# Kernel optimization log

Measured on AMD Instinct MI355X. Metric: run time of the kernel, lower is better.

Reference implementation:

```python
import jax, jax.numpy as jnp
import numpy as np

N = 50000      # n_nodes
E = 800000     # n_edges (nnz)
F = 256        # n_features
H = 256        # architecture (GCN hidden)
K = 16         # n_clusters
CLUSTER_REG = 1.0
CON_REG = 1.0


def setup_inputs() -> dict:
    key = jax.random.key(0)
    ks = jax.random.split(key, 12)
    inp = {
        "edge_src": jax.random.randint(ks[0], (E,), 0, N, dtype=jnp.int32),
        "edge_dst": jax.random.randint(ks[1], (E,), 0, N, dtype=jnp.int32),
        "edge_w_norm": jax.random.uniform(ks[2], (E,), dtype=jnp.float32),
        "features": jax.random.normal(ks[3], (N, F), dtype=jnp.float32),
        "aug_features": jax.random.normal(ks[4], (N, F), dtype=jnp.float32),
        # GCN encoder params (Linear no-bias + additive bias per DGI-style GCN)
        "W1": jax.random.normal(ks[5], (F, H), dtype=jnp.float32) / np.sqrt(F),
        "b1": jnp.zeros((H,), dtype=jnp.float32),
        # student GCN params
        "Ws": jax.random.normal(ks[6], (H, K), dtype=jnp.float32) / np.sqrt(H),
        "bs": jnp.zeros((K,), dtype=jnp.float32),
        # teacher GCN params (EMA copy; fixed here)
        "Wt": jax.random.normal(ks[7], (H, K), dtype=jnp.float32) / np.sqrt(H),
        "bt": jnp.zeros((K,), dtype=jnp.float32),
        "n_nodes": N,
    }
    return inp


def _spmm(w, src, dst, X, n):
    # (sparse A) @ X with A given as COO (src=row, dst=col, w=value)
    return jax.ops.segment_sum(w[:, None] * X[dst], src, num_segments=n)


def _gcn(X, W, b, w, src, dst, n):
    # act(spmm(A_norm, X @ W) + b) with act = selu
    return jax.nn.selu(_spmm(w, src, dst, X @ W, n) + b)


def _normalize(x):
    # F.normalize(x, dim=-1, p=2)
    nrm = jnp.sqrt(jnp.sum(x * x, axis=-1, keepdims=True))
    return x / jnp.maximum(nrm, 1e-12)


def reference(edge_src, edge_dst, edge_w_norm, features, aug_features,
              W1, b1, Ws, bs, Wt, bt, n_nodes):
    n = features.shape[0]
    n_edges = edge_src.shape[0]

    # encoder + student assignments
    gcn_out = _gcn(features, W1, b1, edge_w_norm, edge_src, edge_dst, n)
    logits = _spmm(edge_w_norm, edge_src, edge_dst, gcn_out @ Ws, n) + bs
    assignments = jax.nn.softmax(jax.nn.selu(logits), axis=1)  # [N, K]

    # degrees = torch.sparse.sum(graph, dim=0) (binary adjacency values)
    ones_e = jnp.ones((n_edges,), dtype=features.dtype)
    degrees = jax.ops.segment_sum(ones_e, edge_dst, num_segments=n)[:, None]  # [N,1]

    # graph_pooled = (A @ S).T @ S  (A values are all 1)
    AS = jax.ops.segment_sum(assignments[edge_dst], edge_src, num_segments=n)
    graph_pooled = AS.T @ assignments  # [K, K]

    normalizer_left = assignments.T @ degrees          # [K, 1]
    normalizer = (normalizer_left @ normalizer_left.T) / 2.0 / n_edges
    spectral_loss = -jnp.trace(graph_pooled - normalizer) / 2.0 / n_edges

    cluster_sizes = jnp.sum(assignments, axis=0)
    cluster_loss = (jnp.linalg.norm(cluster_sizes) / n_nodes * np.sqrt(float(K)) - 1.0)
    cluster_loss = cluster_loss * CLUSTER_REG

    # teacher branch (no grad)
    g2 = _gcn(aug_features, W1, b1, edge_w_norm, edge_src, edge_dst, n)
    t_logits = _spmm(edge_w_norm, edge_src, edge_dst, g2 @ Wt, n) + bt
    assignments_hat = jax.lax.stop_gradient(
        jax.nn.softmax(jax.nn.selu(t_logits), axis=-1))

    con = jnp.mean(2.0 - 2.0 * jnp.sum(_normalize(assignments_hat) * _normalize(assignments), axis=-1))

    loss = spectral_loss + cluster_loss + CON_REG * con
    return loss
```

## Files before the change

kernel.cpp:

```cpp
#include <hip/hip_runtime.h>
#include <math.h>

constexpr int Fdim = 256;
constexpr int Hdim = 256;
constexpr int Kc   = 16;

constexpr int RSTRIDE = 32;
constexpr int NRED    = 34;
constexpr int BCAP    = 5120;

typedef __attribute__((ext_vector_type(8))) short s8v;
typedef __attribute__((ext_vector_type(4))) float f4v;

__device__ __forceinline__ float selu1(float x){
    const float scale = 1.0507009873554805f;
    const float alpha = 1.6732632423543772f;
    return scale * (x > 0.f ? x : alpha * expm1f(x));
}

__device__ __forceinline__ ushort f2bf(float x){
    union { float f; unsigned u; } c; c.f = x;
    unsigned r = c.u + 0x7fffu + ((c.u >> 16) & 1u);
    return (ushort)(r >> 16);
}

__device__ __forceinline__ float bflo(unsigned v){
    union { unsigned u; float f; } c; c.u = v << 16; return c.f;
}
__device__ __forceinline__ float bfhi(unsigned v){
    union { unsigned u; float f; } c; c.u = v & 0xffff0000u; return c.f;
}

__device__ __forceinline__ unsigned char f2fp8(float x){
    int v = __builtin_amdgcn_cvt_pk_fp8_f32(x, x, 0, false);
    return (unsigned char)(v & 0xff);
}

__global__ __launch_bounds__(256) void bin_kernel(
        const int* __restrict__ src, const int* __restrict__ dst,
        const float* __restrict__ w,
        int* __restrict__ bcnt,
        int* __restrict__ bsrc, uint2* __restrict__ bdw, int E, int nbuck){
    __shared__ int hist[256];
    __shared__ int base[256];
    __shared__ int cur[256];
    int t = threadIdx.x;
    int chunk = (E + gridDim.x - 1) / gridDim.x;
    int lo = blockIdx.x * chunk;
    int hi = min(lo + chunk, E);
    hist[t] = 0;
    __syncthreads();
    for (int i = lo + t; i < hi; i += 256)
        atomicAdd(&hist[src[i] >> 8], 1);
    __syncthreads();
    if (t < nbuck && hist[t] > 0)
        base[t] = atomicAdd(&bcnt[t * 32], hist[t]);
    cur[t] = 0;
    __syncthreads();
    for (int i = lo + t; i < hi; i += 256){
        int s = src[i], d = dst[i];
        float wv = w[i];
        int b = s >> 8;
        int p = base[b] + atomicAdd(&cur[b], 1);
        if (p < BCAP){
            bsrc[(size_t)b * BCAP + p] = s;
            bdw[(size_t)b * BCAP + p]  = make_uint2((unsigned)d, __float_as_uint(wv));
        }
    }
}

__global__ __launch_bounds__(256) void bbase_kernel(const int* __restrict__ bcnt,
        int* __restrict__ bbase, int* __restrict__ roff, int nbuck, int n){
    __shared__ int s[256];
    int t = threadIdx.x;
    int v = (t < nbuck) ? min(bcnt[t * 32], BCAP) : 0;
    s[t] = v;
    __syncthreads();
    for (int off = 1; off < 256; off <<= 1){
        int x = (t >= off) ? s[t - off] : 0;
        __syncthreads();
        s[t] += x;
        __syncthreads();
    }
    if (t < nbuck) bbase[t] = s[t] - v;
    if (t == 255) roff[n] = s[255];
}

__global__ __launch_bounds__(256) void csr_build_kernel(
        const int* __restrict__ bcnt, const int* __restrict__ bbase,
        const int* __restrict__ bsrc, const uint2* __restrict__ bdw,
        int* __restrict__ roff, uint2* __restrict__ csr, int n){
    __shared__ int hist[256];
    __shared__ int loc[256];
    __shared__ int cur[256];
    int b = blockIdx.x, t = threadIdx.x;
    int cnt  = min(bcnt[b * 32], BCAP);
    int base = bbase[b];
    hist[t] = 0;
    __syncthreads();
    for (int i = t; i < cnt; i += 256)
        atomicAdd(&hist[bsrc[(size_t)b * BCAP + i] & 255], 1);
    __syncthreads();
    int v = hist[t];
    loc[t] = v;
    __syncthreads();
    for (int off = 1; off < 256; off <<= 1){
        int x = (t >= off) ? loc[t - off] : 0;
        __syncthreads();
        loc[t] += x;
        __syncthreads();
    }
    int gi = b * 256 + t;
    if (gi < n) roff[gi] = base + loc[t] - v;
    cur[t] = 0;
    __syncthreads();
    for (int i = t; i < cnt; i += 256){
        int s   = bsrc[(size_t)b * BCAP + i];
        int idx = s & 255;
        int p = base + (loc[idx] - hist[idx]) + atomicAdd(&cur[idx], 1);
        csr[p] = bdw[(size_t)b * BCAP + i];
    }
}

__global__ void castw_kernel(const float* __restrict__ W, ushort* __restrict__ Wt){
    __shared__ float t[16][17];
    int tx = threadIdx.x, ty = threadIdx.y;
    int k  = blockIdx.y * 16 + ty;
    int nn = blockIdx.x * 16 + tx;
    t[ty][tx] = W[k * 256 + nn];
    __syncthreads();
    int n2 = blockIdx.x * 16 + ty;
    int k2 = blockIdx.y * 16 + tx;
    Wt[n2 * 256 + k2] = f2bf(t[tx][ty]);
}

__global__ void castwk_kernel(const float* __restrict__ Ws, const float* __restrict__ Wt,
                              ushort* __restrict__ WsT, ushort* __restrict__ WtT){
    int h = threadIdx.x;
    #pragma unroll
    for (int c = 0; c < 16; ++c){
        WsT[c * 256 + h] = f2bf(Ws[h * 16 + c]);
        WtT[c * 256 + h] = f2bf(Wt[h * 16 + c]);
    }
}

__global__ __launch_bounds__(256, 2) void gemm_xw_kernel(
        const float* __restrict__ A0, const float* __restrict__ A1,
        const ushort* __restrict__ Bt,
        unsigned char* __restrict__ C8, int M){
    __shared__ ushort blds[32768];
    int tid = threadIdx.x;
    int n0  = blockIdx.x * 128;
    int bm  = blockIdx.y * 128;
    const float* A = blockIdx.z ? A1 : A0;
    int halfoff = blockIdx.z * 256;

    #pragma unroll
    for (int j = 0; j < 16; ++j){
        int c  = j * 256 + tid;
        int nl = c >> 5, kc = c & 31;
        uint4 v = *reinterpret_cast<const uint4*>(Bt + (((size_t)(n0 + nl)) << 8) + (kc << 3));
        unsigned boff = (unsigned)(((nl << 9) + (kc << 4)) ^ ((nl & 7) << 4));
        *reinterpret_cast<uint4*>(reinterpret_cast<char*>(blds) + boff) = v;
    }

    int w = tid >> 6, l = tid & 63;
    int lr = l & 15, lk = l >> 4;

    int r0 = bm + w * 32 + lr;
    int r1 = r0 + 16;
    int rc0 = min(r0, M - 1), rc1 = min(r1, M - 1);
    const float* a0 = A + (size_t)rc0 * 256 + lk * 8;
    const float* a1 = A + (size_t)rc1 * 256 + lk * 8;

    float4 f[16], g[16];
    #pragma unroll
    for (int ks = 0; ks < 8; ++ks){
        f[2*ks]   = *reinterpret_cast<const float4*>(a0 + ks * 32);
        f[2*ks+1] = *reinterpret_cast<const float4*>(a0 + ks * 32 + 4);
        g[2*ks]   = *reinterpret_cast<const float4*>(a1 + ks * 32);
        g[2*ks+1] = *reinterpret_cast<const float4*>(a1 + ks * 32 + 4);
    }
    s8v af0[8], af1[8];
    #pragma unroll
    for (int ks = 0; ks < 8; ++ks){
        float4 x0 = f[2*ks], x1 = f[2*ks+1];
        af0[ks][0] = (short)f2bf(x0.x); af0[ks][1] = (short)f2bf(x0.y);
        af0[ks][2] = (short)f2bf(x0.z); af0[ks][3] = (short)f2bf(x0.w);
        af0[ks][4] = (short)f2bf(x1.x); af0[ks][5] = (short)f2bf(x1.y);
        af0[ks][6] = (short)f2bf(x1.z); af0[ks][7] = (short)f2bf(x1.w);
        float4 y0 = g[2*ks], y1 = g[2*ks+1];
        af1[ks][0] = (short)f2bf(y0.x); af1[ks][1] = (short)f2bf(y0.y);
        af1[ks][2] = (short)f2bf(y0.z); af1[ks][3] = (short)f2bf(y0.w);
        af1[ks][4] = (short)f2bf(y1.x); af1[ks][5] = (short)f2bf(y1.y);
        af1[ks][6] = (short)f2bf(y1.z); af1[ks][7] = (short)f2bf(y1.w);
    }
    __syncthreads();

    f4v acc[2][8];
    #pragma unroll
    for (int m = 0; m < 2; ++m)
        #pragma unroll
        for (int t = 0; t < 8; ++t)
            acc[m][t] = (f4v){0.f, 0.f, 0.f, 0.f};

    #pragma unroll
    for (int ks = 0; ks < 8; ++ks){
        #pragma unroll
        for (int t = 0; t < 8; ++t){
            int nl = t * 16 + lr;
            unsigned boff = (unsigned)(((nl << 9) + ((ks * 4 + lk) << 4)) ^ ((nl & 7) << 4));
            s8v bf = *reinterpret_cast<const s8v*>(reinterpret_cast<const char*>(blds) + boff);
            acc[0][t] = __builtin_amdgcn_mfma_f32_16x16x32_bf16(af0[ks], bf, acc[0][t], 0, 0, 0);
            acc[1][t] = __builtin_amdgcn_mfma_f32_16x16x32_bf16(af1[ks], bf, acc[1][t], 0, 0, 0);
        }
    }

    #pragma unroll
    for (int m = 0; m < 2; ++m){
        #pragma unroll
        for (int t = 0; t < 8; ++t){
            int col = n0 + t * 16 + lr;
            #pragma unroll
            for (int j = 0; j < 4; ++j){
                int row = bm + w * 32 + m * 16 + lk * 4 + j;
                if (row < M) C8[(size_t)row * 512 + halfoff + col] = f2fp8(acc[m][t][j]);
            }
        }
    }
}

__global__ __launch_bounds__(256) void spmm_h2_kernel(
        const unsigned char* __restrict__ XWp,
        const int* __restrict__ roff, const uint2* __restrict__ csr,
        const float* __restrict__ b1,
        ushort* __restrict__ Gs, ushort* __restrict__ Gt, int n){
    int wid = threadIdx.x >> 6, lane = threadIdx.x & 63;
    int r = blockIdx.x * 4 + wid;
    if (r >= n) return;
    int half = lane >> 5;
    int hl   = lane & 31;
    const unsigned char* base = XWp + lane * 8;
    int e0 = roff[r], e1 = roff[r + 1];
    float acc[8] = {};

    #define ACCUM8(V, W) do{                                                      \
        auto fa_ = __builtin_amdgcn_cvt_pk_f32_fp8((V).x, false);                 \
        acc[0] = fmaf((W), fa_[0], acc[0]); acc[1] = fmaf((W), fa_[1], acc[1]);   \
        auto fb_ = __builtin_amdgcn_cvt_pk_f32_fp8((V).x, true);                  \
        acc[2] = fmaf((W), fb_[0], acc[2]); acc[3] = fmaf((W), fb_[1], acc[3]);   \
        auto fc_ = __builtin_amdgcn_cvt_pk_f32_fp8((V).y, false);                 \
        acc[4] = fmaf((W), fc_[0], acc[4]); acc[5] = fmaf((W), fc_[1], acc[5]);   \
        auto fd_ = __builtin_amdgcn_cvt_pk_f32_fp8((V).y, true);                  \
        acc[6] = fmaf((W), fd_[0], acc[6]); acc[7] = fmaf((W), fd_[1], acc[7]);   \
    }while(0)

    int e = e0;
    for (; e + 7 < e1; e += 8){
        uint2 c0 = csr[e],     c1 = csr[e + 1];
        uint2 c2 = csr[e + 2], c3 = csr[e + 3];
        uint2 c4 = csr[e + 4], c5 = csr[e + 5];
        uint2 c6 = csr[e + 6], c7 = csr[e + 7];
        uint2 v0 = *reinterpret_cast<const uint2*>(base + ((size_t)c0.x << 9));
        uint2 v1 = *reinterpret_cast<const uint2*>(base + ((size_t)c1.x << 9));
        uint2 v2 = *reinterpret_cast<const uint2*>(base + ((size_t)c2.x << 9));
        uint2 v3 = *reinterpret_cast<const uint2*>(base + ((size_t)c3.x << 9));
        uint2 v4 = *reinterpret_cast<const uint2*>(base + ((size_t)c4.x << 9));
        uint2 v5 = *reinterpret_cast<const uint2*>(base + ((size_t)c5.x << 9));
        uint2 v6 = *reinterpret_cast<const uint2*>(base + ((size_t)c6.x << 9));
        uint2 v7 = *reinterpret_cast<const uint2*>(base + ((size_t)c7.x << 9));
        ACCUM8(v0, __uint_as_float(c0.y)); ACCUM8(v1, __uint_as_float(c1.y));
        ACCUM8(v2, __uint_as_float(c2.y)); ACCUM8(v3, __uint_as_float(c3.y));
        ACCUM8(v4, __uint_as_float(c4.y)); ACCUM8(v5, __uint_as_float(c5.y));
        ACCUM8(v6, __uint_as_float(c6.y)); ACCUM8(v7, __uint_as_float(c7.y));
    }
    for (; e + 3 < e1; e += 4){
        uint2 c0 = csr[e],     c1 = csr[e + 1];
        uint2 c2 = csr[e + 2], c3 = csr[e + 3];
        uint2 v0 = *reinterpret_cast<const uint2*>(base + ((size_t)c0.x << 9));
        uint2 v1 = *reinterpret_cast<const uint2*>(base + ((size_t)c1.x << 9));
        uint2 v2 = *reinterpret_cast<const uint2*>(base + ((size_t)c2.x << 9));
        uint2 v3 = *reinterpret_cast<const uint2*>(base + ((size_t)c3.x << 9));
        ACCUM8(v0, __uint_as_float(c0.y)); ACCUM8(v1, __uint_as_float(c1.y));
        ACCUM8(v2, __uint_as_float(c2.y)); ACCUM8(v3, __uint_as_float(c3.y));
    }
    for (; e < e1; ++e){
        uint2 c = csr[e];
        uint2 v = *reinterpret_cast<const uint2*>(base + ((size_t)c.x << 9));
        ACCUM8(v, __uint_as_float(c.y));
    }
    #undef ACCUM8

    const float* bp = b1 + hl * 8;
    float4 bb0 = *reinterpret_cast<const float4*>(bp);
    float4 bb1 = *reinterpret_cast<const float4*>(bp + 4);
    float bv[8] = {bb0.x, bb0.y, bb0.z, bb0.w, bb1.x, bb1.y, bb1.z, bb1.w};
    ushort o[8];
    #pragma unroll
    for (int q = 0; q < 8; ++q) o[q] = f2bf(selu1(acc[q] + bv[q]));
    uint4 ov = *reinterpret_cast<const uint4*>(o);
    ushort* gout = (half ? Gt : Gs) + (size_t)r * Hdim + hl * 8;
    *reinterpret_cast<uint4*>(gout) = ov;
}

__global__ __launch_bounds__(256) void gemm_k2_kernel(
        const ushort* __restrict__ Gs, const ushort* __restrict__ Gt,
        const ushort* __restrict__ WsT, const ushort* __restrict__ WtT,
        unsigned* __restrict__ GSp, int n){
    int wv = blockIdx.x * 4 + (threadIdx.x >> 6);
    int l  = threadIdx.x & 63;
    int lr = l & 15, lk = l >> 4;
    int nw = (n + 15) >> 4;
    if (wv >= nw) return;
    int r0 = wv * 16;

    s8v bs_[8], bt_[8];
    #pragma unroll
    for (int ks = 0; ks < 8; ++ks){
        bs_[ks] = *reinterpret_cast<const s8v*>(WsT + lr * 256 + ks * 32 + lk * 8);
        bt_[ks] = *reinterpret_cast<const s8v*>(WtT + lr * 256 + ks * 32 + lk * 8);
    }

    f4v accs = (f4v){0.f,0.f,0.f,0.f}, acct = (f4v){0.f,0.f,0.f,0.f};
    int row = min(r0 + lr, n - 1);
    const ushort* gsrow = Gs + (size_t)row * 256 + lk * 8;
    const ushort* gtrow = Gt + (size_t)row * 256 + lk * 8;
    #pragma unroll
    for (int ks = 0; ks < 8; ++ks){
        s8v a_s = *reinterpret_cast<const s8v*>(gsrow + ks * 32);
        s8v a_t = *reinterpret_cast<const s8v*>(gtrow + ks * 32);
        accs = __builtin_amdgcn_mfma_f32_16x16x32_bf16(a_s, bs_[ks], accs, 0, 0, 0);
        acct = __builtin_amdgcn_mfma_f32_16x16x32_bf16(a_t, bt_[ks], acct, 0, 0, 0);
    }
    #pragma unroll
    for (int j = 0; j < 4; ++j){
        int rr = r0 + lk * 4 + j;
        if (rr < n){
            unsigned pv = (unsigned)f2bf(accs[j]) | ((unsigned)f2bf(acct[j]) << 16);
            GSp[(size_t)rr * 16 + lr] = pv;
        }
    }
}

__global__ __launch_bounds__(256) void spmm_k2_kernel(
        const unsigned* __restrict__ GSp,
        const int* __restrict__ roff, const uint2* __restrict__ csr,
        const float* __restrict__ bsv, const float* __restrict__ btv,
        float* __restrict__ asg, float* __restrict__ red, int n){
    int tid  = threadIdx.x;
    int wid  = tid >> 6, lane = tid & 63;
    int slot = lane >> 4, j = lane & 15;
    float bs_ = bsv[j], bt_ = btv[j];
    float cs_l = 0.f, con_l = 0.f;

    int rstride = gridDim.x * 4;
    for (int r = blockIdx.x * 4 + wid; r < n; r += rstride){
        int e0 = roff[r], e1 = roff[r + 1];
        float as_ = 0.f, at_ = 0.f;
        for (int e = e0 + slot; e < e1; e += 4){
            uint2 c = csr[e];
            float w = __uint_as_float(c.y);
            unsigned v = GSp[(size_t)c.x * 16 + j];
            as_ = fmaf(w, bflo(v), as_);
            at_ = fmaf(w, bfhi(v), at_);
        }
        as_ += __shfl_xor(as_, 16); as_ += __shfl_xor(as_, 32);
        at_ += __shfl_xor(at_, 16); at_ += __shfl_xor(at_, 32);
        float xs = selu1(as_ + bs_);
        float xt = selu1(at_ + bt_);
        float ms = xs, mt = xt;
        #pragma unroll
        for (int off = 8; off >= 1; off >>= 1){
            ms = fmaxf(ms, __shfl_xor(ms, off));
            mt = fmaxf(mt, __shfl_xor(mt, off));
        }
        float es = expf(xs - ms), et = expf(xt - mt);
        float ss = es, st = et;
        #pragma unroll
        for (int off = 8; off >= 1; off >>= 1){
            ss += __shfl_xor(ss, off);
            st += __shfl_xor(st, off);
        }
        float a = es / ss, b = et / st;
        if (slot == 0) asg[(size_t)r * 16 + j] = a;
        cs_l += a;
        float dot = a * b, na = a * a, nb = b * b;
        #pragma unroll
        for (int off = 8; off >= 1; off >>= 1){
            dot += __shfl_xor(dot, off);
            na  += __shfl_xor(na, off);
            nb  += __shfl_xor(nb, off);
        }
        if (j == 0){
            na = fmaxf(sqrtf(na), 1e-12f);
            nb = fmaxf(sqrtf(nb), 1e-12f);
            con_l += 2.f - 2.f * dot / (na * nb);
        }
    }

    cs_l  += __shfl_xor(cs_l, 16);  cs_l  += __shfl_xor(cs_l, 32);  cs_l  *= 0.25f;
    con_l += __shfl_xor(con_l, 16); con_l += __shfl_xor(con_l, 32); con_l *= 0.25f;

    __shared__ float part[4][17];
    if (lane < 16) part[wid][lane] = cs_l;
    if (lane == 0) part[wid][16]   = con_l;
    __syncthreads();
    if (tid < 16){
        float s = part[0][tid] + part[1][tid] + part[2][tid] + part[3][tid];
        atomicAdd(&red[(16 + tid) * RSTRIDE], s);
    } else if (tid == 16){
        float s = part[0][16] + part[1][16] + part[2][16] + part[3][16];
        atomicAdd(&red[32 * RSTRIDE], s);
    }
}

__global__ __launch_bounds__(256) void edge_trace_kernel(const int* __restrict__ src,
        const int* __restrict__ dst, const float* __restrict__ as_,
        float* __restrict__ red, int E){
    int tid    = blockIdx.x * blockDim.x + threadIdx.x;
    int stride = gridDim.x * blockDim.x;
    float dot = 0.f;
    float nl[16] = {};
    for (int i = tid; i < E; i += stride){
        const float4* pa = reinterpret_cast<const float4*>(as_ + (size_t)src[i] * 16);
        const float4* pb = reinterpret_cast<const float4*>(as_ + (size_t)dst[i] * 16);
        #pragma unroll
        for (int q = 0; q < 4; ++q){
            float4 va = pa[q]; float4 vb = pb[q];
            dot = fmaf(va.x, vb.x, dot); dot = fmaf(va.y, vb.y, dot);
            dot = fmaf(va.z, vb.z, dot); dot = fmaf(va.w, vb.w, dot);
            nl[q*4+0] += vb.x; nl[q*4+1] += vb.y;
            nl[q*4+2] += vb.z; nl[q*4+3] += vb.w;
        }
    }
    #pragma unroll
    for (int off = 1; off < 64; off <<= 1){
        dot += __shfl_xor(dot, off);
        #pragma unroll
        for (int k = 0; k < 16; ++k) nl[k] += __shfl_xor(nl[k], off);
    }
    __shared__ float part[4][17];
    int wid = threadIdx.x >> 6, lane = threadIdx.x & 63;
    if (lane == 0){
        #pragma unroll
        for (int k = 0; k < 16; ++k) part[wid][k] = nl[k];
        part[wid][16] = dot;
    }
    __syncthreads();
    int t = threadIdx.x;
    if (t < 16){
        float s = part[0][t] + part[1][t] + part[2][t] + part[3][t];
        atomicAdd(&red[t * RSTRIDE], s);
    } else if (t == 16){
        float s = part[0][16] + part[1][16] + part[2][16] + part[3][16];
        atomicAdd(&red[33 * RSTRIDE], s);
    }
}

__global__ void finalize_kernel(const float* __restrict__ red, float* __restrict__ out,
                                int n, int E){
    float trace = red[33 * RSTRIDE];
    float nl2 = 0.f, cs2 = 0.f;
    #pragma unroll
    for (int k = 0; k < 16; ++k){
        nl2 = fmaf(red[k * RSTRIDE],        red[k * RSTRIDE],        nl2);
        cs2 = fmaf(red[(16 + k) * RSTRIDE], red[(16 + k) * RSTRIDE], cs2);
    }
    float twoE = 2.f * (float)E;
    float spectral = -(trace - nl2 / twoE) / twoE;
    float cluster  = sqrtf(cs2) / (float)n * 4.f - 1.f;
    float con      = red[32 * RSTRIDE] / (float)n;
    out[0] = spectral + cluster + con;
}

extern "C" void kernel_launch(void* const* d_in, const int* in_sizes, int n_in,
                              void* d_out, int out_size, void* d_ws, size_t ws_size,
                              hipStream_t stream){
    const int*   esrc = (const int*)d_in[0];
    const int*   edst = (const int*)d_in[1];
    const float* ew   = (const float*)d_in[2];
    const float* feat = (const float*)d_in[3];
    const float* faug = (const float*)d_in[4];
    const float* W1   = (const float*)d_in[5];
    const float* b1   = (const float*)d_in[6];
    const float* Wsm  = (const float*)d_in[7];
    const float* bsv  = (const float*)d_in[8];
    const float* Wtm  = (const float*)d_in[9];
    const float* btv  = (const float*)d_in[10];
    int E = in_sizes[0];
    int N = in_sizes[3] / Fdim;

    char* ws = (char*)d_ws;
    size_t off = 0;
    auto alloc = [&](size_t bytes) -> char* {
        char* p = ws + off;
        off = (off + bytes + 255) & ~(size_t)255;
        return p;
    };
    int nbuck = (N + 255) >> 8;
    unsigned char* XWp = (unsigned char*)alloc((size_t)N * 512);
    ushort*   Gs    = (ushort*)alloc((size_t)N * Hdim * 2);
    ushort*   Gt    = (ushort*)alloc((size_t)N * Hdim * 2);
    unsigned* GSp   = (unsigned*)alloc((size_t)N * Kc * 4);
    float*    ASG_S = (float*)alloc((size_t)N * Kc * 4);
    ushort*   WT    = (ushort*)alloc((size_t)256 * 256 * 2);
    ushort*   WsT   = (ushort*)alloc((size_t)16 * 256 * 2);
    ushort*   WtT   = (ushort*)alloc((size_t)16 * 256 * 2);
    int*      ROFF  = (int*)alloc((size_t)(N + 1) * 4);
    int*      BBASE = (int*)alloc((size_t)(nbuck + 1) * 4);
    int*      BCNT  = (int*)alloc((size_t)nbuck * 32 * 4);
    int*      BSRC  = (int*)alloc((size_t)nbuck * BCAP * 4);
    uint2*    BDW   = (uint2*)alloc((size_t)nbuck * BCAP * 8);
    uint2*    CSR8  = (uint2*)alloc((size_t)E * 8);
    float*    RED   = (float*)alloc((size_t)NRED * RSTRIDE * 4);

    hipMemsetAsync(BCNT, 0, (size_t)nbuck * 32 * 4, stream);
    hipMemsetAsync(RED, 0, (size_t)NRED * RSTRIDE * 4, stream);

    castw_kernel<<<dim3(16, 16), dim3(16, 16), 0, stream>>>(W1, WT);
    castwk_kernel<<<1, 256, 0, stream>>>(Wsm, Wtm, WsT, WtT);
    bin_kernel<<<256, 256, 0, stream>>>(esrc, edst, ew, BCNT, BSRC, BDW, E, nbuck);
    bbase_kernel<<<1, 256, 0, stream>>>(BCNT, BBASE, ROFF, nbuck, N);
    csr_build_kernel<<<nbuck, 256, 0, stream>>>(BCNT, BBASE, BSRC, BDW, ROFF, CSR8, N);

    dim3 gg(2, (N + 127) / 128, 2);
    gemm_xw_kernel<<<gg, 256, 0, stream>>>(feat, faug, WT, XWp, N);

    spmm_h2_kernel<<<(N + 3) / 4, 256, 0, stream>>>(XWp, ROFF, CSR8, b1, Gs, Gt, N);

    int nw = (N + 15) / 16;
    gemm_k2_kernel<<<(nw + 3) / 4, 256, 0, stream>>>(Gs, Gt, WsT, WtT, GSp, N);

    spmm_k2_kernel<<<2048, 256, 0, stream>>>(GSp, ROFF, CSR8, bsv, btv,
                                             ASG_S, RED, N);

    edge_trace_kernel<<<256, 256, 0, stream>>>(esrc, edst, ASG_S, RED, E);
    finalize_kernel<<<1, 1, 0, stream>>>(RED, (float*)d_out, N, E);
}
```

Before: 245.9 us.

## Split GEMM K-loop to halve LDS, use packed FMA and nontemporal CSR loads

The XW GEMM now stages B in two K halves, which halves the LDS buffer and register-held A fragments, and raises launch bounds to 4 blocks per CU for higher occupancy. This adds an extra barrier and serialises the load and compute phases within each block. The first SpMM switches its accumulators to 2-wide float vectors so the compiler can emit packed FMAs. Both SpMM kernels read CSR entries with nontemporal 64-bit loads, and the first one writes its output with nontemporal stores to reduce cache pollution.

```diff
diff --git a/kernel.cpp b/kernel.cpp
--- a/kernel.cpp
+++ b/kernel.cpp
@@ -11,6 +11,8 @@
 
 typedef __attribute__((ext_vector_type(8))) short s8v;
 typedef __attribute__((ext_vector_type(4))) float f4v;
+typedef __attribute__((ext_vector_type(2))) float f2v;
+typedef __attribute__((ext_vector_type(4))) unsigned u4v;
 
 __device__ __forceinline__ float selu1(float x){
     const float scale = 1.0507009873554805f;
@@ -144,58 +146,23 @@
     }
 }
 
-__global__ __launch_bounds__(256, 2) void gemm_xw_kernel(
+__global__ __launch_bounds__(256, 4) void gemm_xw_kernel(
         const float* __restrict__ A0, const float* __restrict__ A1,
         const ushort* __restrict__ Bt,
         unsigned char* __restrict__ C8, int M){
-    __shared__ ushort blds[32768];
+    __shared__ ushort blds[16384];
     int tid = threadIdx.x;
     int n0  = blockIdx.x * 128;
     int bm  = blockIdx.y * 128;
     const float* A = blockIdx.z ? A1 : A0;
     int halfoff = blockIdx.z * 256;
 
-    #pragma unroll
-    for (int j = 0; j < 16; ++j){
-        int c  = j * 256 + tid;
-        int nl = c >> 5, kc = c & 31;
-        uint4 v = *reinterpret_cast<const uint4*>(Bt + (((size_t)(n0 + nl)) << 8) + (kc << 3));
-        unsigned boff = (unsigned)(((nl << 9) + (kc << 4)) ^ ((nl & 7) << 4));
-        *reinterpret_cast<uint4*>(reinterpret_cast<char*>(blds) + boff) = v;
-    }
-
     int w = tid >> 6, l = tid & 63;
     int lr = l & 15, lk = l >> 4;
 
     int r0 = bm + w * 32 + lr;
     int r1 = r0 + 16;
     int rc0 = min(r0, M - 1), rc1 = min(r1, M - 1);
-    const float* a0 = A + (size_t)rc0 * 256 + lk * 8;
-    const float* a1 = A + (size_t)rc1 * 256 + lk * 8;
-
-    float4 f[16], g[16];
-    #pragma unroll
-    for (int ks = 0; ks < 8; ++ks){
-        f[2*ks]   = *reinterpret_cast<const float4*>(a0 + ks * 32);
-        f[2*ks+1] = *reinterpret_cast<const float4*>(a0 + ks * 32 + 4);
-        g[2*ks]   = *reinterpret_cast<const float4*>(a1 + ks * 32);
-        g[2*ks+1] = *reinterpret_cast<const float4*>(a1 + ks * 32 + 4);
-    }
-    s8v af0[8], af1[8];
-    #pragma unroll
-    for (int ks = 0; ks < 8; ++ks){
-        float4 x0 = f[2*ks], x1 = f[2*ks+1];
-        af0[ks][0] = (short)f2bf(x0.x); af0[ks][1] = (short)f2bf(x0.y);
-        af0[ks][2] = (short)f2bf(x0.z); af0[ks][3] = (short)f2bf(x0.w);
-        af0[ks][4] = (short)f2bf(x1.x); af0[ks][5] = (short)f2bf(x1.y);
-        af0[ks][6] = (short)f2bf(x1.z); af0[ks][7] = (short)f2bf(x1.w);
-        float4 y0 = g[2*ks], y1 = g[2*ks+1];
-        af1[ks][0] = (short)f2bf(y0.x); af1[ks][1] = (short)f2bf(y0.y);
-        af1[ks][2] = (short)f2bf(y0.z); af1[ks][3] = (short)f2bf(y0.w);
-        af1[ks][4] = (short)f2bf(y1.x); af1[ks][5] = (short)f2bf(y1.y);
-        af1[ks][6] = (short)f2bf(y1.z); af1[ks][7] = (short)f2bf(y1.w);
-    }
-    __syncthreads();
 
     f4v acc[2][8];
     #pragma unroll
@@ -204,16 +171,49 @@
         for (int t = 0; t < 8; ++t)
             acc[m][t] = (f4v){0.f, 0.f, 0.f, 0.f};
 
-    #pragma unroll
-    for (int ks = 0; ks < 8; ++ks){
-        #pragma unroll
-        for (int t = 0; t < 8; ++t){
-            int nl = t * 16 + lr;
-            unsigned boff = (unsigned)(((nl << 9) + ((ks * 4 + lk) << 4)) ^ ((nl & 7) << 4));
-            s8v bf = *reinterpret_cast<const s8v*>(reinterpret_cast<const char*>(blds) + boff);
-            acc[0][t] = __builtin_amdgcn_mfma_f32_16x16x32_bf16(af0[ks], bf, acc[0][t], 0, 0, 0);
-            acc[1][t] = __builtin_amdgcn_mfma_f32_16x16x32_bf16(af1[ks], bf, acc[1][t], 0, 0, 0);
-        }
+    for (int kp = 0; kp < 2; ++kp){
+        #pragma unroll
+        for (int j = 0; j < 8; ++j){
+            int c  = j * 256 + tid;
+            int nl = c >> 4, kc = c & 15;
+            uint4 v = *reinterpret_cast<const uint4*>(
+                Bt + (((size_t)(n0 + nl)) << 8) + kp * 128 + (kc << 3));
+            unsigned boff = (unsigned)(((nl << 8) + (kc << 4)) ^ ((nl & 7) << 4));
+            *reinterpret_cast<uint4*>(reinterpret_cast<char*>(blds) + boff) = v;
+        }
+
+        const float* a0 = A + (size_t)rc0 * 256 + kp * 128 + lk * 8;
+        const float* a1 = A + (size_t)rc1 * 256 + kp * 128 + lk * 8;
+        s8v af0[4], af1[4];
+        #pragma unroll
+        for (int ks = 0; ks < 4; ++ks){
+            float4 x0 = *reinterpret_cast<const float4*>(a0 + ks * 32);
+            float4 x1 = *reinterpret_cast<const float4*>(a0 + ks * 32 + 4);
+            af0[ks][0] = (short)f2bf(x0.x); af0[ks][1] = (short)f2bf(x0.y);
+            af0[ks][2] = (short)f2bf(x0.z); af0[ks][3] = (short)f2bf(x0.w);
+            af0[ks][4] = (short)f2bf(x1.x); af0[ks][5] = (short)f2bf(x1.y);
+            af0[ks][6] = (short)f2bf(x1.z); af0[ks][7] = (short)f2bf(x1.w);
+            float4 y0 = *reinterpret_cast<const float4*>(a1 + ks * 32);
+            float4 y1 = *reinterpret_cast<const float4*>(a1 + ks * 32 + 4);
+            af1[ks][0] = (short)f2bf(y0.x); af1[ks][1] = (short)f2bf(y0.y);
+            af1[ks][2] = (short)f2bf(y0.z); af1[ks][3] = (short)f2bf(y0.w);
+            af1[ks][4] = (short)f2bf(y1.x); af1[ks][5] = (short)f2bf(y1.y);
+            af1[ks][6] = (short)f2bf(y1.z); af1[ks][7] = (short)f2bf(y1.w);
+        }
+        __syncthreads();
+
+        #pragma unroll
+        for (int ks = 0; ks < 4; ++ks){
+            #pragma unroll
+            for (int t = 0; t < 8; ++t){
+                int nl = t * 16 + lr;
+                unsigned boff = (unsigned)(((nl << 8) + ((ks * 4 + lk) << 4)) ^ ((nl & 7) << 4));
+                s8v bf = *reinterpret_cast<const s8v*>(reinterpret_cast<const char*>(blds) + boff);
+                acc[0][t] = __builtin_amdgcn_mfma_f32_16x16x32_bf16(af0[ks], bf, acc[0][t], 0, 0, 0);
+                acc[1][t] = __builtin_amdgcn_mfma_f32_16x16x32_bf16(af1[ks], bf, acc[1][t], 0, 0, 0);
+            }
+        }
+        if (kp == 0) __syncthreads();
     }
 
     #pragma unroll
@@ -241,53 +241,51 @@
     int half = lane >> 5;
     int hl   = lane & 31;
     const unsigned char* base = XWp + lane * 8;
+    const unsigned long long* csr8 = reinterpret_cast<const unsigned long long*>(csr);
     int e0 = roff[r], e1 = roff[r + 1];
-    float acc[8] = {};
-
-    #define ACCUM8(V, W) do{                                                      \
-        auto fa_ = __builtin_amdgcn_cvt_pk_f32_fp8((V).x, false);                 \
-        acc[0] = fmaf((W), fa_[0], acc[0]); acc[1] = fmaf((W), fa_[1], acc[1]);   \
-        auto fb_ = __builtin_amdgcn_cvt_pk_f32_fp8((V).x, true);                  \
-        acc[2] = fmaf((W), fb_[0], acc[2]); acc[3] = fmaf((W), fb_[1], acc[3]);   \
-        auto fc_ = __builtin_amdgcn_cvt_pk_f32_fp8((V).y, false);                 \
-        acc[4] = fmaf((W), fc_[0], acc[4]); acc[5] = fmaf((W), fc_[1], acc[5]);   \
-        auto fd_ = __builtin_amdgcn_cvt_pk_f32_fp8((V).y, true);                  \
-        acc[6] = fmaf((W), fd_[0], acc[6]); acc[7] = fmaf((W), fd_[1], acc[7]);   \
+    f2v acc2[4] = {(f2v){0.f,0.f}, (f2v){0.f,0.f}, (f2v){0.f,0.f}, (f2v){0.f,0.f}};
+
+    #define ACCUM8(V, W) do{                                          \
+        f2v w2_ = (f2v){(W), (W)};                                    \
+        f2v fa_ = __builtin_amdgcn_cvt_pk_f32_fp8((V).x, false);      \
+        f2v fb_ = __builtin_amdgcn_cvt_pk_f32_fp8((V).x, true);       \
+        f2v fc_ = __builtin_amdgcn_cvt_pk_f32_fp8((V).y, false);      \
+        f2v fd_ = __builtin_amdgcn_cvt_pk_f32_fp8((V).y, true);       \
+        acc2[0] += w2_ * fa_; acc2[1] += w2_ * fb_;                   \
+        acc2[2] += w2_ * fc_; acc2[3] += w2_ * fd_;                   \
     }while(0)
 
     int e = e0;
     for (; e + 7 < e1; e += 8){
-        uint2 c0 = csr[e],     c1 = csr[e + 1];
-        uint2 c2 = csr[e + 2], c3 = csr[e + 3];
-        uint2 c4 = csr[e + 4], c5 = csr[e + 5];
-        uint2 c6 = csr[e + 6], c7 = csr[e + 7];
-        uint2 v0 = *reinterpret_cast<const uint2*>(base + ((size_t)c0.x << 9));
-        uint2 v1 = *reinterpret_cast<const uint2*>(base + ((size_t)c1.x << 9));
-        uint2 v2 = *reinterpret_cast<const uint2*>(base + ((size_t)c2.x << 9));
-        uint2 v3 = *reinterpret_cast<const uint2*>(base + ((size_t)c3.x << 9));
-        uint2 v4 = *reinterpret_cast<const uint2*>(base + ((size_t)c4.x << 9));
-        uint2 v5 = *reinterpret_cast<const uint2*>(base + ((size_t)c5.x << 9));
-        uint2 v6 = *reinterpret_cast<const uint2*>(base + ((size_t)c6.x << 9));
-        uint2 v7 = *reinterpret_cast<const uint2*>(base + ((size_t)c7.x << 9));
-        ACCUM8(v0, __uint_as_float(c0.y)); ACCUM8(v1, __uint_as_float(c1.y));
-        ACCUM8(v2, __uint_as_float(c2.y)); ACCUM8(v3, __uint_as_float(c3.y));
-        ACCUM8(v4, __uint_as_float(c4.y)); ACCUM8(v5, __uint_as_float(c5.y));
-        ACCUM8(v6, __uint_as_float(c6.y)); ACCUM8(v7, __uint_as_float(c7.y));
-    }
-    for (; e + 3 < e1; e += 4){
-        uint2 c0 = csr[e],     c1 = csr[e + 1];
-        uint2 c2 = csr[e + 2], c3 = csr[e + 3];
-        uint2 v0 = *reinterpret_cast<const uint2*>(base + ((size_t)c0.x << 9));
-        uint2 v1 = *reinterpret_cast<const uint2*>(base + ((size_t)c1.x << 9));
-        uint2 v2 = *reinterpret_cast<const uint2*>(base + ((size_t)c2.x << 9));
-        uint2 v3 = *reinterpret_cast<const uint2*>(base + ((size_t)c3.x << 9));
-        ACCUM8(v0, __uint_as_float(c0.y)); ACCUM8(v1, __uint_as_float(c1.y));
-        ACCUM8(v2, __uint_as_float(c2.y)); ACCUM8(v3, __uint_as_float(c3.y));
+        unsigned long long q0 = __builtin_nontemporal_load(csr8 + e);
+        unsigned long long q1 = __builtin_nontemporal_load(csr8 + e + 1);
+        unsigned long long q2 = __builtin_nontemporal_load(csr8 + e + 2);
+        unsigned long long q3 = __builtin_nontemporal_load(csr8 + e + 3);
+        unsigned long long q4 = __builtin_nontemporal_load(csr8 + e + 4);
+        unsigned long long q5 = __builtin_nontemporal_load(csr8 + e + 5);
+        unsigned long long q6 = __builtin_nontemporal_load(csr8 + e + 6);
+        unsigned long long q7 = __builtin_nontemporal_load(csr8 + e + 7);
+        uint2 v0 = *reinterpret_cast<const uint2*>(base + ((size_t)(unsigned)q0 << 9));
+        uint2 v1 = *reinterpret_cast<const uint2*>(base + ((size_t)(unsigned)q1 << 9));
+        uint2 v2 = *reinterpret_cast<const uint2*>(base + ((size_t)(unsigned)q2 << 9));
+        uint2 v3 = *reinterpret_cast<const uint2*>(base + ((size_t)(unsigned)q3 << 9));
+        uint2 v4 = *reinterpret_cast<const uint2*>(base + ((size_t)(unsigned)q4 << 9));
+        uint2 v5 = *reinterpret_cast<const uint2*>(base + ((size_t)(unsigned)q5 << 9));
+        uint2 v6 = *reinterpret_cast<const uint2*>(base + ((size_t)(unsigned)q6 << 9));
+        uint2 v7 = *reinterpret_cast<const uint2*>(base + ((size_t)(unsigned)q7 << 9));
+        ACCUM8(v0, __uint_as_float((unsigned)(q0 >> 32)));
+        ACCUM8(v1, __uint_as_float((unsigned)(q1 >> 32)));
+        ACCUM8(v2, __uint_as_float((unsigned)(q2 >> 32)));
+        ACCUM8(v3, __uint_as_float((unsigned)(q3 >> 32)));
+        ACCUM8(v4, __uint_as_float((unsigned)(q4 >> 32)));
+        ACCUM8(v5, __uint_as_float((unsigned)(q5 >> 32)));
+        ACCUM8(v6, __uint_as_float((unsigned)(q6 >> 32)));
+        ACCUM8(v7, __uint_as_float((unsigned)(q7 >> 32)));
     }
     for (; e < e1; ++e){
-        uint2 c = csr[e];
-        uint2 v = *reinterpret_cast<const uint2*>(base + ((size_t)c.x << 9));
-        ACCUM8(v, __uint_as_float(c.y));
+        unsigned long long q = __builtin_nontemporal_load(csr8 + e);
+        uint2 v = *reinterpret_cast<const uint2*>(base + ((size_t)(unsigned)q << 9));
+        ACCUM8(v, __uint_as_float((unsigned)(q >> 32)));
     }
     #undef ACCUM8
 
@@ -297,10 +295,13 @@
     float bv[8] = {bb0.x, bb0.y, bb0.z, bb0.w, bb1.x, bb1.y, bb1.z, bb1.w};
     ushort o[8];
     #pragma unroll
-    for (int q = 0; q < 8; ++q) o[q] = f2bf(selu1(acc[q] + bv[q]));
-    uint4 ov = *reinterpret_cast<const uint4*>(o);
+    for (int i = 0; i < 4; ++i){
+        o[2*i]   = f2bf(selu1(acc2[i][0] + bv[2*i]));
+        o[2*i+1] = f2bf(selu1(acc2[i][1] + bv[2*i+1]));
+    }
+    u4v ov = *reinterpret_cast<const u4v*>(o);
     ushort* gout = (half ? Gt : Gs) + (size_t)r * Hdim + hl * 8;
-    *reinterpret_cast<uint4*>(gout) = ov;
+    __builtin_nontemporal_store(ov, reinterpret_cast<u4v*>(gout));
 }
 
 __global__ __launch_bounds__(256) void gemm_k2_kernel(
@@ -350,6 +351,7 @@
     int tid  = threadIdx.x;
     int wid  = tid >> 6, lane = tid & 63;
     int slot = lane >> 4, j = lane & 15;
+    const unsigned long long* csr8 = reinterpret_cast<const unsigned long long*>(csr);
     float bs_ = bsv[j], bt_ = btv[j];
     float cs_l = 0.f, con_l = 0.f;
 
@@ -358,9 +360,9 @@
         int e0 = roff[r], e1 = roff[r + 1];
         float as_ = 0.f, at_ = 0.f;
         for (int e = e0 + slot; e < e1; e += 4){
-            uint2 c = csr[e];
-            float w = __uint_as_float(c.y);
-            unsigned v = GSp[(size_t)c.x * 16 + j];
+            unsigned long long q = __builtin_nontemporal_load(csr8 + e);
+            float w = __uint_as_float((unsigned)(q >> 32));
+            unsigned v = GSp[(size_t)(unsigned)q * 16 + j];
             as_ = fmaf(w, bflo(v), as_);
             at_ = fmaf(w, bfhi(v), at_);
         }
```

After: 346.8 us. 1.41x slower.
